# Kernel optimization log

Hardware: AMD Instinct MI355X
Metric: run time of the kernel (lower is better)

Reference implementation:

```python
import jax, jax.numpy as jnp
import numpy as np

EMB = 1024
HEADS = 16
BLOCK = 128


def setup_inputs() -> dict:
    key = jax.random.key(0)
    k1, k2, k3 = jax.random.split(key, 3)
    B, T, C = 4, 4096, EMB
    x = jax.random.normal(k1, (B, T, C), dtype=jnp.float32)
    # Linear weights stored as [in, out] (i.e. torch W.T); qkv has no bias.
    W_qkv = jax.random.normal(k2, (C, 3 * C), dtype=jnp.float32) * 0.02
    W_proj = jax.random.normal(k3, (C, C), dtype=jnp.float32) * 0.02
    b_proj = jnp.zeros((C,), dtype=jnp.float32)
    return {"x": x, "W_qkv": W_qkv, "W_proj": W_proj, "b_proj": b_proj}


def reference(x, W_qkv, W_proj, b_proj):
    # Dropout is inference-mode identity.
    B, T, C = x.shape
    H, D, BS = HEADS, C // HEADS, BLOCK
    nb = T // BS  # number of local blocks
    qkv = x @ W_qkv  # [B,T,3C]
    q, k, v = jnp.split(qkv, 3, axis=-1)
    # [B, nb, BS, H, D] -- each block attends only within itself
    q = q.reshape(B, nb, BS, H, D)
    k = k.reshape(B, nb, BS, H, D)
    v = v.reshape(B, nb, BS, H, D)
    scores = jnp.einsum("bnqhd,bnkhd->bnhqk", q, k) / jnp.sqrt(jnp.float32(D))
    # is_decoder: causal tril within each diagonal block (tril[i:end, i:end])
    tril = jnp.tril(jnp.ones((BS, BS), dtype=bool))
    scores = jnp.where(tril, scores, -jnp.inf)
    # faithful to original: stable exp, then divide by (sum + 1e-6)
    scores = scores - jnp.max(scores, axis=-1, keepdims=True)
    e = jnp.exp(scores)
    p = e / (jnp.sum(e, axis=-1, keepdims=True) + 1e-6)
    out = jnp.einsum("bnhqk,bnkhd->bnqhd", p, v).reshape(B, T, C)
    return out @ W_proj + b_proj
```

## Files before the change

kernel.cpp:

```cpp
#include <hip/hip_runtime.h>
#include <hip/hip_bf16.h>
#include <math.h>


typedef __bf16 bf16_t;
typedef __bf16 bf16x8 __attribute__((ext_vector_type(8)));
typedef float  f32x4  __attribute__((ext_vector_type(4)));

typedef const __attribute__((address_space(1))) void* gptr_t;
typedef __attribute__((address_space(3))) void* lptr_t;

__global__ __launch_bounds__(256) void cvt_f32_bf16(const float* __restrict__ in,
                                                    bf16_t* __restrict__ out, size_t n) {
    size_t stride = (size_t)gridDim.x * blockDim.x * 4;
    for (size_t i = ((size_t)blockIdx.x * blockDim.x + threadIdx.x) * 4; i < n; i += stride) {
        float4 v = *(const float4*)(in + i);
        bf16_t t[4];
        t[0] = (bf16_t)v.x; t[1] = (bf16_t)v.y; t[2] = (bf16_t)v.z; t[3] = (bf16_t)v.w;
        *(uint2*)(out + i) = *(uint2*)t;
    }
}

__global__ __launch_bounds__(256) void transpose_cvt(const float* __restrict__ in,
                                                     bf16_t* __restrict__ out, int K, int N) {
    __shared__ float tile[32][33];
    const int tx = threadIdx.x & 31, ty = threadIdx.x >> 5;
    const int bx = blockIdx.x, by = blockIdx.y;
    #pragma unroll
    for (int i = 0; i < 4; i++) {
        const int k = by * 32 + ty + i * 8;
        tile[ty + i * 8][tx] = in[(size_t)k * N + bx * 32 + tx];
    }
    __syncthreads();
    #pragma unroll
    for (int i = 0; i < 4; i++) {
        const int n = bx * 32 + ty + i * 8;
        out[(size_t)n * K + by * 32 + tx] = (bf16_t)tile[tx][ty + i * 8];
    }
}

template <bool BF16_OUT, bool BIAS>
__global__ __launch_bounds__(512, 2) void gemm256(const bf16_t* __restrict__ A,
                                                  const bf16_t* __restrict__ Bt,
                                                  void* __restrict__ Cout,
                                                  const float* __restrict__ bias,
                                                  int M, int N, int K) {
    __shared__ bf16_t As[2][256 * 64];
    __shared__ bf16_t Bs[2][256 * 64];

    const int tid  = threadIdx.x;
    const int lane = tid & 63, wave = tid >> 6;
    const int quad = lane >> 4, l16 = lane & 15;
    const int wm = wave >> 2, wn = wave & 3;
    const int bn = blockIdx.x, bm = blockIdx.y;

    const bf16_t* Ab = A  + (size_t)bm * 256 * K;
    const bf16_t* Bb = Bt + (size_t)bn * 256 * K;

    const int r0  = tid >> 3;
    const int c8s = (tid & 7) ^ (r0 & 7);
    const int swz = l16 & 7;

    f32x4 acc[8][4];
    #pragma unroll
    for (int i = 0; i < 8; ++i)
        #pragma unroll
        for (int j = 0; j < 4; ++j) acc[i][j] = (f32x4){0.f, 0.f, 0.f, 0.f};

#define STAGE(DST, SRC, H, I, KOFF)                                                   \
    __builtin_amdgcn_global_load_lds(                                                 \
        (gptr_t)((SRC) + (size_t)((H) * 128 + (I) * 64 + r0) * K + (KOFF) + c8s * 8), \
        (lptr_t)&(DST)[(H) * 8192 + (I) * 4096 + wave * 512], 16, 0, 0)

    STAGE(As[0], Ab, 0, 0, 0); STAGE(As[0], Ab, 0, 1, 0);
    STAGE(As[0], Ab, 1, 0, 0); STAGE(As[0], Ab, 1, 1, 0);
    STAGE(Bs[0], Bb, 0, 0, 0); STAGE(Bs[0], Bb, 0, 1, 0);
    STAGE(Bs[0], Bb, 1, 0, 0); STAGE(Bs[0], Bb, 1, 1, 0);
    __syncthreads();

    const int NT = K >> 6;
    for (int t = 0; t < NT; ++t) {
        const int cur = t & 1;
        const bool pf = (t + 1) < NT;
        const int kk = (t + 1) << 6;
        bf16_t* Asn = As[cur ^ 1];
        bf16_t* Bsn = Bs[cur ^ 1];
        const bf16_t* Asc = As[cur];
        const bf16_t* Bsc = Bs[cur];

        #pragma unroll
        for (int q = 0; q < 4; ++q) {
            const int mh = q >> 1, nh = q & 1;

            bf16x8 af[4][2], bf[2][2];
            #pragma unroll
            for (int mr = 0; mr < 4; ++mr) {
                const int arow = wm * 128 + (mh * 4 + mr) * 16 + l16;
                #pragma unroll
                for (int ks = 0; ks < 2; ++ks)
                    af[mr][ks] = *(const bf16x8*)&Asc[arow * 64 + ((((ks << 2) | quad) ^ swz) << 3)];
            }
            #pragma unroll
            for (int nr = 0; nr < 2; ++nr) {
                const int brow = wn * 64 + (nh * 2 + nr) * 16 + l16;
                #pragma unroll
                for (int ks = 0; ks < 2; ++ks)
                    bf[nr][ks] = *(const bf16x8*)&Bsc[brow * 64 + ((((ks << 2) | quad) ^ swz) << 3)];
            }

            if (q == 0 && pf) {
                STAGE(Asn, Ab, 0, 0, kk); STAGE(Asn, Ab, 0, 1, kk);
                STAGE(Asn, Ab, 1, 0, kk); STAGE(Asn, Ab, 1, 1, kk);
            }
            if (q == 1 && pf) {
                STAGE(Bsn, Bb, 0, 0, kk); STAGE(Bsn, Bb, 0, 1, kk);
                STAGE(Bsn, Bb, 1, 0, kk); STAGE(Bsn, Bb, 1, 1, kk);
            }

            __builtin_amdgcn_s_barrier();
            __builtin_amdgcn_s_setprio(1);
            #pragma unroll
            for (int mr = 0; mr < 4; ++mr)
                #pragma unroll
                for (int nr = 0; nr < 2; ++nr)
                    #pragma unroll
                    for (int ks = 0; ks < 2; ++ks)
                        acc[mh * 4 + mr][nh * 2 + nr] = __builtin_amdgcn_mfma_f32_16x16x32_bf16(
                            af[mr][ks], bf[nr][ks], acc[mh * 4 + mr][nh * 2 + nr], 0, 0, 0);
            __builtin_amdgcn_s_setprio(0);

            if (q < 3)
                __builtin_amdgcn_s_barrier();
            else
                __syncthreads();
        }
    }
#undef STAGE

    #pragma unroll
    for (int mr = 0; mr < 8; ++mr) {
        #pragma unroll
        for (int nr = 0; nr < 4; ++nr) {
            const int gcol = bn * 256 + wn * 64 + nr * 16 + l16;
            #pragma unroll
            for (int reg = 0; reg < 4; ++reg) {
                const int grow = bm * 256 + wm * 128 + mr * 16 + quad * 4 + reg;
                float v = acc[mr][nr][reg];
                if (BIAS) v += bias[gcol];
                if (BF16_OUT)
                    ((bf16_t*)Cout)[(size_t)grow * N + gcol] = (bf16_t)v;
                else
                    ((float*)Cout)[(size_t)grow * N + gcol] = v;
            }
        }
    }
}

__global__ __launch_bounds__(256, 3) void attn_kernel(const bf16_t* __restrict__ qkv,
                                                      bf16_t* __restrict__ attn_out) {
    __shared__ __align__(16) char smem[54272];
    bf16_t* qs = (bf16_t*)smem;
    bf16_t* ks = (bf16_t*)(smem + 18432);
    bf16_t* vT = (bf16_t*)(smem + 36864);
    bf16_t* ps = (bf16_t*)smem;

    const int tid = threadIdx.x;
    const int lane = tid & 63, wave = tid >> 6;
    const int quad = lane >> 4, l16 = lane & 15;

    const int bid = blockIdx.x;
    const int h = bid & 15;
    const int blk = (bid >> 4) & 31;
    const int b = bid >> 9;
    const int row0 = (b * 32 + blk) * 128;
    const int LDQ = 3072;

    for (int t = tid; t < 128 * 8; t += 256) {
        const int r = t >> 3;
        const int c = (t & 7) * 8;
        const bf16_t* src = qkv + (size_t)(row0 + r) * LDQ + h * 64;
        *(uint4*)&qs[r * 72 + c] = *(const uint4*)(src + c);
        *(uint4*)&ks[r * 72 + c] = *(const uint4*)(src + 1024 + c);
        bf16x8 vv = *(const bf16x8*)(src + 2048 + c);
        #pragma unroll
        for (int j = 0; j < 8; j++)
            vT[(c + j) * 136 + r] = vv[j];
    }
    __syncthreads();

    f32x4 sfrag[2][8];
    for (int mr = 0; mr < 2; mr++)
        for (int nc = 0; nc < 8; nc++)
            sfrag[mr][nc] = (f32x4){0.f, 0.f, 0.f, 0.f};

    #pragma unroll
    for (int ksl = 0; ksl < 2; ksl++) {
        bf16x8 aq[2], bk[8];
        #pragma unroll
        for (int mr = 0; mr < 2; mr++)
            aq[mr] = *(const bf16x8*)&qs[(wave * 32 + mr * 16 + l16) * 72 + ksl * 32 + quad * 8];
        #pragma unroll
        for (int nc = 0; nc < 8; nc++)
            bk[nc] = *(const bf16x8*)&ks[(nc * 16 + l16) * 72 + ksl * 32 + quad * 8];
        #pragma unroll
        for (int mr = 0; mr < 2; mr++)
            #pragma unroll
            for (int nc = 0; nc < 8; nc++)
                sfrag[mr][nc] = __builtin_amdgcn_mfma_f32_16x16x32_bf16(aq[mr], bk[nc], sfrag[mr][nc], 0, 0, 0);
    }

    #pragma unroll
    for (int mr = 0; mr < 2; mr++) {
        #pragma unroll
        for (int nc = 0; nc < 8; nc++) {
            #pragma unroll
            for (int reg = 0; reg < 4; reg++) {
                const int row = wave * 32 + mr * 16 + quad * 4 + reg;
                const int col = nc * 16 + l16;
                float s = sfrag[mr][nc][reg] * 0.125f;
                if (col > row) s = -INFINITY;
                sfrag[mr][nc][reg] = s;
            }
        }
    }

    #pragma unroll
    for (int mr = 0; mr < 2; mr++) {
        #pragma unroll
        for (int reg = 0; reg < 4; reg++) {
            float m = -INFINITY;
            #pragma unroll
            for (int nc = 0; nc < 8; nc++) m = fmaxf(m, sfrag[mr][nc][reg]);
            #pragma unroll
            for (int off = 1; off < 16; off <<= 1) m = fmaxf(m, __shfl_xor(m, off));
            float sum = 0.f;
            #pragma unroll
            for (int nc = 0; nc < 8; nc++) {
                float e = __expf(sfrag[mr][nc][reg] - m);
                sfrag[mr][nc][reg] = e;
                sum += e;
            }
            #pragma unroll
            for (int off = 1; off < 16; off <<= 1) sum += __shfl_xor(sum, off);
            const float inv = 1.0f / (sum + 1e-6f);
            #pragma unroll
            for (int nc = 0; nc < 8; nc++) sfrag[mr][nc][reg] *= inv;
        }
    }

    __syncthreads();

    #pragma unroll
    for (int mr = 0; mr < 2; mr++)
        #pragma unroll
        for (int nc = 0; nc < 8; nc++)
            #pragma unroll
            for (int reg = 0; reg < 4; reg++) {
                const int row = wave * 32 + mr * 16 + quad * 4 + reg;
                const int col = nc * 16 + l16;
                ps[row * 136 + col] = (bf16_t)sfrag[mr][nc][reg];
            }
    __syncthreads();

    f32x4 oacc[2][4];
    for (int mr = 0; mr < 2; mr++)
        for (int nd = 0; nd < 4; nd++)
            oacc[mr][nd] = (f32x4){0.f, 0.f, 0.f, 0.f};

    #pragma unroll
    for (int ksl = 0; ksl < 4; ksl++) {
        bf16x8 ap[2];
        #pragma unroll
        for (int mr = 0; mr < 2; mr++)
            ap[mr] = *(const bf16x8*)&ps[(wave * 32 + mr * 16 + l16) * 136 + ksl * 32 + quad * 8];
        #pragma unroll
        for (int nd = 0; nd < 4; nd++) {
            bf16x8 bv = *(const bf16x8*)&vT[(nd * 16 + l16) * 136 + ksl * 32 + quad * 8];
            #pragma unroll
            for (int mr = 0; mr < 2; mr++)
                oacc[mr][nd] = __builtin_amdgcn_mfma_f32_16x16x32_bf16(ap[mr], bv, oacc[mr][nd], 0, 0, 0);
        }
    }

    #pragma unroll
    for (int mr = 0; mr < 2; mr++)
        #pragma unroll
        for (int nd = 0; nd < 4; nd++)
            #pragma unroll
            for (int reg = 0; reg < 4; reg++) {
                const int row = row0 + wave * 32 + mr * 16 + quad * 4 + reg;
                const int col = h * 64 + nd * 16 + l16;
                attn_out[(size_t)row * 1024 + col] = (bf16_t)oacc[mr][nd][reg];
            }
}

extern "C" void kernel_launch(void* const* d_in, const int* in_sizes, int n_in,
                              void* d_out, int out_size, void* d_ws, size_t ws_size,
                              hipStream_t stream) {
    const float* x     = (const float*)d_in[0];
    const float* Wqkv  = (const float*)d_in[1];
    const float* Wproj = (const float*)d_in[2];
    const float* bproj = (const float*)d_in[3];

    const int M = 16384, C = 1024, N1 = 3072;

    char* ws = (char*)d_ws;
    bf16_t* xb     = (bf16_t*)(ws);
    bf16_t* wqkvT  = (bf16_t*)(ws + 33554432);
    bf16_t* wprojT = (bf16_t*)(ws + 39845888);
    bf16_t* qkvb   = (bf16_t*)(ws + 41943040);
    bf16_t* attnb  = (bf16_t*)(ws + 142606336);

    cvt_f32_bf16<<<8192, 256, 0, stream>>>(x, xb, (size_t)M * C);
    transpose_cvt<<<dim3(N1 / 32, C / 32), 256, 0, stream>>>(Wqkv, wqkvT, C, N1);
    transpose_cvt<<<dim3(C / 32, C / 32), 256, 0, stream>>>(Wproj, wprojT, C, C);

    gemm256<true, false><<<dim3(N1 / 256, M / 256), 512, 0, stream>>>(
        xb, wqkvT, (void*)qkvb, nullptr, M, N1, C);

    attn_kernel<<<2048, 256, 0, stream>>>(qkvb, attnb);

    gemm256<false, true><<<dim3(C / 256, M / 256), 512, 0, stream>>>(
        attnb, wprojT, d_out, bproj, M, C, C);
}
```

Measured before the change: 324.9 us.

## Restructure GEMM main loop into 4-slot K=32 pipeline with vmcnt waits

Replaces the double-buffered K=64 tile loop in the bf16 GEMM with a four-slot ring of K=32 slices that are prefetched three steps ahead. Explicit s_waitcnt vmcnt counts plus a single barrier per slice replace the per-quarter barriers and full __syncthreads. The shared-memory swizzle changes to suit the narrower 32-element rows. The aim is deeper load/compute overlap and fewer barriers, at the risk of more bank conflicts on the 64-byte rows and fragile hand-counted vmcnt values.

```diff
diff --git a/kernel.cpp b/kernel.cpp
--- a/kernel.cpp
+++ b/kernel.cpp
@@ -45,8 +45,8 @@
                                                   void* __restrict__ Cout,
                                                   const float* __restrict__ bias,
                                                   int M, int N, int K) {
-    __shared__ bf16_t As[2][256 * 64];
-    __shared__ bf16_t Bs[2][256 * 64];
+    __shared__ bf16_t As[4][256 * 32];
+    __shared__ bf16_t Bs[4][256 * 32];
 
     const int tid  = threadIdx.x;
     const int lane = tid & 63, wave = tid >> 6;
@@ -57,9 +57,9 @@
     const bf16_t* Ab = A  + (size_t)bm * 256 * K;
     const bf16_t* Bb = Bt + (size_t)bn * 256 * K;
 
-    const int r0  = tid >> 3;
-    const int c8s = (tid & 7) ^ (r0 & 7);
-    const int swz = l16 & 7;
+    const int srow = lane >> 2;
+    const int scs  = (lane & 3) ^ ((srow >> 1) & 3);
+    const int csw  = (l16 >> 1) & 3;
 
     f32x4 acc[8][4];
     #pragma unroll
@@ -67,75 +67,66 @@
         #pragma unroll
         for (int j = 0; j < 4; ++j) acc[i][j] = (f32x4){0.f, 0.f, 0.f, 0.f};
 
-#define STAGE(DST, SRC, H, I, KOFF)                                                   \
+#define STG(ARR, SRC, SLOT, SLICE, I)                                                 \
     __builtin_amdgcn_global_load_lds(                                                 \
-        (gptr_t)((SRC) + (size_t)((H) * 128 + (I) * 64 + r0) * K + (KOFF) + c8s * 8), \
-        (lptr_t)&(DST)[(H) * 8192 + (I) * 4096 + wave * 512], 16, 0, 0)
-
-    STAGE(As[0], Ab, 0, 0, 0); STAGE(As[0], Ab, 0, 1, 0);
-    STAGE(As[0], Ab, 1, 0, 0); STAGE(As[0], Ab, 1, 1, 0);
-    STAGE(Bs[0], Bb, 0, 0, 0); STAGE(Bs[0], Bb, 0, 1, 0);
-    STAGE(Bs[0], Bb, 1, 0, 0); STAGE(Bs[0], Bb, 1, 1, 0);
-    __syncthreads();
-
-    const int NT = K >> 6;
-    for (int t = 0; t < NT; ++t) {
-        const int cur = t & 1;
-        const bool pf = (t + 1) < NT;
-        const int kk = (t + 1) << 6;
-        bf16_t* Asn = As[cur ^ 1];
-        bf16_t* Bsn = Bs[cur ^ 1];
-        const bf16_t* Asc = As[cur];
-        const bf16_t* Bsc = Bs[cur];
-
-        #pragma unroll
-        for (int q = 0; q < 4; ++q) {
-            const int mh = q >> 1, nh = q & 1;
-
-            bf16x8 af[4][2], bf[2][2];
-            #pragma unroll
-            for (int mr = 0; mr < 4; ++mr) {
-                const int arow = wm * 128 + (mh * 4 + mr) * 16 + l16;
-                #pragma unroll
-                for (int ks = 0; ks < 2; ++ks)
-                    af[mr][ks] = *(const bf16x8*)&Asc[arow * 64 + ((((ks << 2) | quad) ^ swz) << 3)];
-            }
-            #pragma unroll
-            for (int nr = 0; nr < 2; ++nr) {
-                const int brow = wn * 64 + (nh * 2 + nr) * 16 + l16;
-                #pragma unroll
-                for (int ks = 0; ks < 2; ++ks)
-                    bf[nr][ks] = *(const bf16x8*)&Bsc[brow * 64 + ((((ks << 2) | quad) ^ swz) << 3)];
-            }
-
-            if (q == 0 && pf) {
-                STAGE(Asn, Ab, 0, 0, kk); STAGE(Asn, Ab, 0, 1, kk);
-                STAGE(Asn, Ab, 1, 0, kk); STAGE(Asn, Ab, 1, 1, kk);
-            }
-            if (q == 1 && pf) {
-                STAGE(Bsn, Bb, 0, 0, kk); STAGE(Bsn, Bb, 0, 1, kk);
-                STAGE(Bsn, Bb, 1, 0, kk); STAGE(Bsn, Bb, 1, 1, kk);
-            }
-
-            __builtin_amdgcn_s_barrier();
-            __builtin_amdgcn_s_setprio(1);
-            #pragma unroll
-            for (int mr = 0; mr < 4; ++mr)
-                #pragma unroll
-                for (int nr = 0; nr < 2; ++nr)
-                    #pragma unroll
-                    for (int ks = 0; ks < 2; ++ks)
-                        acc[mh * 4 + mr][nh * 2 + nr] = __builtin_amdgcn_mfma_f32_16x16x32_bf16(
-                            af[mr][ks], bf[nr][ks], acc[mh * 4 + mr][nh * 2 + nr], 0, 0, 0);
-            __builtin_amdgcn_s_setprio(0);
-
-            if (q < 3)
-                __builtin_amdgcn_s_barrier();
-            else
-                __syncthreads();
-        }
-    }
-#undef STAGE
+        (gptr_t)((SRC) + (size_t)(wave * 32 + (I) * 16 + srow) * K + (SLICE) * 32 +   \
+                 scs * 8),                                                            \
+        (lptr_t)&(ARR)[SLOT][(wave * 32 + (I) * 16) * 32], 16, 0, 0)
+
+#define STAGE4(SLICE)                                                                 \
+    do {                                                                              \
+        const int sl_ = (SLICE) & 3;                                                  \
+        STG(As, Ab, sl_, SLICE, 0); STG(As, Ab, sl_, SLICE, 1);                       \
+        STG(Bs, Bb, sl_, SLICE, 0); STG(Bs, Bb, sl_, SLICE, 1);                       \
+    } while (0)
+
+#define COMPUTE(KS)                                                                   \
+    do {                                                                              \
+        const bf16_t* Asl_ = As[(KS) & 3];                                            \
+        const bf16_t* Bsl_ = Bs[(KS) & 3];                                            \
+        bf16x8 af_[8], bf_[4];                                                        \
+        _Pragma("unroll")                                                             \
+        for (int fr = 0; fr < 8; ++fr)                                                \
+            af_[fr] = *(const bf16x8*)&Asl_[(wm * 128 + fr * 16 + l16) * 32 +         \
+                                            ((quad ^ csw) << 3)];                     \
+        _Pragma("unroll")                                                             \
+        for (int fr = 0; fr < 4; ++fr)                                                \
+            bf_[fr] = *(const bf16x8*)&Bsl_[(wn * 64 + fr * 16 + l16) * 32 +          \
+                                            ((quad ^ csw) << 3)];                     \
+        __builtin_amdgcn_s_setprio(1);                                                \
+        _Pragma("unroll")                                                             \
+        for (int mr = 0; mr < 8; ++mr)                                                \
+            _Pragma("unroll")                                                         \
+            for (int nr = 0; nr < 4; ++nr)                                            \
+                acc[mr][nr] = __builtin_amdgcn_mfma_f32_16x16x32_bf16(                \
+                    af_[mr], bf_[nr], acc[mr][nr], 0, 0, 0);                          \
+        __builtin_amdgcn_s_setprio(0);                                                \
+    } while (0)
+
+    #pragma unroll
+    for (int s = 0; s < 3; ++s) STAGE4(s);
+
+    const int NS = K >> 5;
+    for (int ks = 0; ks < NS - 3; ++ks) {
+        asm volatile("s_waitcnt vmcnt(8)" ::: "memory");
+        __builtin_amdgcn_s_barrier();
+        STAGE4(ks + 3);
+        COMPUTE(ks);
+    }
+    {
+        asm volatile("s_waitcnt vmcnt(8)" ::: "memory");
+        __builtin_amdgcn_s_barrier();
+        COMPUTE(NS - 3);
+        asm volatile("s_waitcnt vmcnt(4)" ::: "memory");
+        __builtin_amdgcn_s_barrier();
+        COMPUTE(NS - 2);
+        asm volatile("s_waitcnt vmcnt(0)" ::: "memory");
+        __builtin_amdgcn_s_barrier();
+        COMPUTE(NS - 1);
+    }
+#undef COMPUTE
+#undef STAGE4
+#undef STG
 
     #pragma unroll
     for (int mr = 0; mr < 8; ++mr) {
```

Measured after the change: 347.4 us. 6.9% more time.
